# Performance work log

Hardware: AMD Instinct MI355X
Metric: run time of the kernel (lower is better)

## Reference

```python
import jax, jax.numpy as jnp
import numpy as np

N = 16384
D = 256


def setup_inputs() -> dict:
    key = jax.random.key(0)
    k1, k2, k3, k4 = jax.random.split(key, 4)
    x = jax.random.normal(k1, (N, D), dtype=jnp.float32)
    adj = jax.random.randint(k2, (N, N), 0, 2, dtype=jnp.int32)  # dense 0/1 adjacency
    W = jax.random.normal(k3, (D, D), dtype=jnp.float32) * 0.05
    b = jax.random.normal(k4, (D,), dtype=jnp.float32) * 0.05
    return {"x": x, "adj": adj, "W": W, "b": b}


def reference(x, adj, W, b):
    # neighbors of node i are columns where adj[i, :] == 1; mean-aggregate then Linear
    a = (adj == 1).astype(x.dtype)               # [N, N]
    deg = jnp.sum(a, axis=1, keepdims=True)      # [N, 1]
    agg = jnp.einsum('ij,jf->if', a, x) / deg    # mean over neighbors, [N, D]
    return agg @ W.T + b                         # nn.Linear(in, out)
```

## Files before the change

kernel.cpp:

```cpp
#include <hip/hip_runtime.h>
#include <stdint.h>

typedef __attribute__((ext_vector_type(8))) short shortx8;
typedef __attribute__((ext_vector_type(4))) float floatx4;

#define NR 16384
#define DD 256
#define SA 72
#define NSPLIT 4
#define KCH (NR / NSPLIT)
#define BK 64
#define NIT (KCH / BK)

__device__ __forceinline__ unsigned short f2bf(float f) {
    union { float f; uint32_t u; } v; v.f = f;
    uint32_t u = v.u;
    return (unsigned short)((u + 0x7FFFu + ((u >> 16) & 1u)) >> 16);
}

__global__ __launch_bounds__(256) void k_xpose(const float* __restrict__ x,
                                               unsigned short* __restrict__ xT) {
    __shared__ unsigned short t[64][72];
    const int kb = blockIdx.x * 64;
    const int nb = blockIdx.y * 64;
    const int tid = threadIdx.x;
    const int lr = tid >> 4;
    const int lc = (tid & 15) * 4;
#pragma unroll
    for (int i = 0; i < 4; ++i) {
        const int k = kb + lr + 16 * i;
        const float4 v = *(const float4*)(x + (size_t)k * DD + nb + lc);
        t[lc + 0][lr + 16 * i] = f2bf(v.x);
        t[lc + 1][lr + 16 * i] = f2bf(v.y);
        t[lc + 2][lr + 16 * i] = f2bf(v.z);
        t[lc + 3][lr + 16 * i] = f2bf(v.w);
    }
    __syncthreads();
#pragma unroll
    for (int i = 0; i < 4; ++i) {
        const int nl = lr + 16 * i;
        ushort4 o;
        o.x = t[nl][lc + 0]; o.y = t[nl][lc + 1];
        o.z = t[nl][lc + 2]; o.w = t[nl][lc + 3];
        *(ushort4*)(xT + (size_t)(nb + nl) * NR + kb + lc) = o;
    }
}

__global__ __launch_bounds__(256, 3) void k_agg(const int* __restrict__ adj,
                                                const unsigned short* __restrict__ xT,
                                                float* __restrict__ aggP,
                                                float* __restrict__ degP) {
    __shared__ __align__(16) unsigned short As[64 * SA];
    __shared__ __align__(16) unsigned short Bs[256 * SA];
    __shared__ int degs[64];

    const int tid  = threadIdx.x;
    const int wave = tid >> 6;
    const int lane = tid & 63;
    const int q    = lane >> 4;
    const int ln   = lane & 15;
    const int m0   = blockIdx.x * 64;
    const int kb0  = blockIdx.y * KCH;

    if (tid < 64) degs[tid] = 0;

    const int arow = tid >> 4;
    const int acol = (tid & 15) * 4;

    const int* ap0 = adj + (size_t)(m0 + arow) * NR + kb0 + acol;
    const int* ap1 = ap0 + (size_t)16 * NR;
    const int* ap2 = ap0 + (size_t)32 * NR;
    const int* ap3 = ap0 + (size_t)48 * NR;

    const unsigned short* bg[9];
    unsigned short* const blb = Bs + wave * 9 * 512;
#pragma unroll
    for (int j = 0; j < 9; ++j) {
        const int cid = (wave * 9 + j) * 64 + lane;
        const int n = cid / 9;
        int c = cid - n * 9; if (c > 7) c = 7;
        bg[j] = xT + (size_t)n * NR + kb0 + c * 8;
    }

    floatx4 acc[4][4] = {};
    int dacc0 = 0, dacc1 = 0, dacc2 = 0, dacc3 = 0;

    int4 a0 = *(const int4*)ap0;
    int4 a1 = *(const int4*)ap1;
    int4 a2 = *(const int4*)ap2;
    int4 a3 = *(const int4*)ap3;

    for (int it = 0; it < NIT; ++it) {
        __syncthreads();

#pragma unroll
        for (int j = 0; j < 9; ++j) {
            __builtin_amdgcn_global_load_lds(
                (const __attribute__((address_space(1))) void*)bg[j],
                (__attribute__((address_space(3))) void*)(blb + j * 512),
                16, 0, 0);
            bg[j] += BK;
        }

        ushort4 w;
        w.x = a0.x ? 0x3F80 : 0; w.y = a0.y ? 0x3F80 : 0;
        w.z = a0.z ? 0x3F80 : 0; w.w = a0.w ? 0x3F80 : 0;
        *(ushort4*)&As[(arow +  0) * SA + acol] = w;
        dacc0 += a0.x + a0.y + a0.z + a0.w;

        w.x = a1.x ? 0x3F80 : 0; w.y = a1.y ? 0x3F80 : 0;
        w.z = a1.z ? 0x3F80 : 0; w.w = a1.w ? 0x3F80 : 0;
        *(ushort4*)&As[(arow + 16) * SA + acol] = w;
        dacc1 += a1.x + a1.y + a1.z + a1.w;

        w.x = a2.x ? 0x3F80 : 0; w.y = a2.y ? 0x3F80 : 0;
        w.z = a2.z ? 0x3F80 : 0; w.w = a2.w ? 0x3F80 : 0;
        *(ushort4*)&As[(arow + 32) * SA + acol] = w;
        dacc2 += a2.x + a2.y + a2.z + a2.w;

        w.x = a3.x ? 0x3F80 : 0; w.y = a3.y ? 0x3F80 : 0;
        w.z = a3.z ? 0x3F80 : 0; w.w = a3.w ? 0x3F80 : 0;
        *(ushort4*)&As[(arow + 48) * SA + acol] = w;
        dacc3 += a3.x + a3.y + a3.z + a3.w;

        __syncthreads();

        if (it + 1 < NIT) {
            ap0 += BK; ap1 += BK; ap2 += BK; ap3 += BK;
            a0 = *(const int4*)ap0;
            a1 = *(const int4*)ap1;
            a2 = *(const int4*)ap2;
            a3 = *(const int4*)ap3;
        }

#pragma unroll
        for (int ks = 0; ks < 2; ++ks) {
            const int kk = ks * 32 + q * 8;
            shortx8 af[4], bf[4];
#pragma unroll
            for (int mt = 0; mt < 4; ++mt)
                af[mt] = *(const shortx8*)&As[(mt * 16 + ln) * SA + kk];
#pragma unroll
            for (int nt = 0; nt < 4; ++nt)
                bf[nt] = *(const shortx8*)&Bs[(wave * 64 + nt * 16 + ln) * SA + kk];
#pragma unroll
            for (int mt = 0; mt < 4; ++mt)
#pragma unroll
                for (int nt = 0; nt < 4; ++nt)
                    acc[mt][nt] = __builtin_amdgcn_mfma_f32_16x16x32_bf16(
                        af[mt], bf[nt], acc[mt][nt], 0, 0, 0);
        }
    }

    atomicAdd(&degs[arow +  0], dacc0);
    atomicAdd(&degs[arow + 16], dacc1);
    atomicAdd(&degs[arow + 32], dacc2);
    atomicAdd(&degs[arow + 48], dacc3);
    __syncthreads();
    if (tid < 64) degP[(size_t)blockIdx.y * NR + m0 + tid] = (float)degs[tid];

    float* const outb = aggP + (size_t)blockIdx.y * NR * DD;
#pragma unroll
    for (int mt = 0; mt < 4; ++mt)
#pragma unroll
        for (int nt = 0; nt < 4; ++nt)
#pragma unroll
            for (int r = 0; r < 4; ++r) {
                const int row = m0 + mt * 16 + q * 4 + r;
                const int col = wave * 64 + nt * 16 + ln;
                outb[(size_t)row * DD + col] = acc[mt][nt][r];
            }
}

__global__ __launch_bounds__(256, 2) void k_lin(const float* __restrict__ aggP,
                                                const float* __restrict__ degP,
                                                const float* __restrict__ W,
                                                const float* __restrict__ bias,
                                                float* __restrict__ out) {
    __shared__ __align__(16) unsigned short As[64 * SA];
    __shared__ __align__(16) unsigned short Bs[256 * SA];
    __shared__ float rdeg[64];
    __shared__ float bsh[256];

    const int tid  = threadIdx.x;
    const int wave = tid >> 6;
    const int lane = tid & 63;
    const int q    = lane >> 4;
    const int ln   = lane & 15;
    const int m0   = blockIdx.x * 64;

    if (tid < 64) {
        float d = 0.f;
#pragma unroll
        for (int s = 0; s < NSPLIT; ++s) d += degP[(size_t)s * NR + m0 + tid];
        rdeg[tid] = 1.0f / d;
    }
    bsh[tid] = bias[tid];

    const int arow = tid >> 4;
    const int acol = (tid & 15) * 4;

    floatx4 acc[4][4] = {};

    for (int it = 0; it < 4; ++it) {
        const int kb = it * 64;
        __syncthreads();

#pragma unroll
        for (int i = 0; i < 4; ++i) {
            const int r = arow + 16 * i;
            const size_t g = (size_t)(m0 + r) * DD + kb + acol;
            float4 p = *(const float4*)(aggP + g);
#pragma unroll
            for (int s = 1; s < NSPLIT; ++s) {
                const float4 ps = *(const float4*)(aggP + (size_t)s * NR * DD + g);
                p.x += ps.x; p.y += ps.y; p.z += ps.z; p.w += ps.w;
            }
            const float sc = rdeg[r];
            ushort4 o;
            o.x = f2bf(p.x * sc);
            o.y = f2bf(p.y * sc);
            o.z = f2bf(p.z * sc);
            o.w = f2bf(p.w * sc);
            *(ushort4*)&As[r * SA + acol] = o;
        }
#pragma unroll
        for (int i = 0; i < 16; ++i) {
            const int r = arow + 16 * i;
            const float4 w4 = *(const float4*)(W + (size_t)r * DD + kb + acol);
            ushort4 o;
            o.x = f2bf(w4.x); o.y = f2bf(w4.y);
            o.z = f2bf(w4.z); o.w = f2bf(w4.w);
            *(ushort4*)&Bs[r * SA + acol] = o;
        }
        __syncthreads();

#pragma unroll
        for (int ks = 0; ks < 2; ++ks) {
            const int kk = ks * 32 + q * 8;
            shortx8 af[4], bf[4];
#pragma unroll
            for (int mt = 0; mt < 4; ++mt)
                af[mt] = *(const shortx8*)&As[(mt * 16 + ln) * SA + kk];
#pragma unroll
            for (int nt = 0; nt < 4; ++nt)
                bf[nt] = *(const shortx8*)&Bs[(wave * 64 + nt * 16 + ln) * SA + kk];
#pragma unroll
            for (int mt = 0; mt < 4; ++mt)
#pragma unroll
                for (int nt = 0; nt < 4; ++nt)
                    acc[mt][nt] = __builtin_amdgcn_mfma_f32_16x16x32_bf16(
                        af[mt], bf[nt], acc[mt][nt], 0, 0, 0);
        }
    }

#pragma unroll
    for (int mt = 0; mt < 4; ++mt)
#pragma unroll
        for (int nt = 0; nt < 4; ++nt)
#pragma unroll
            for (int r = 0; r < 4; ++r) {
                const int row = m0 + mt * 16 + q * 4 + r;
                const int col = wave * 64 + nt * 16 + ln;
                out[(size_t)row * DD + col] = acc[mt][nt][r] + bsh[col];
            }
}

extern "C" void kernel_launch(void* const* d_in, const int* in_sizes, int n_in,
                              void* d_out, int out_size, void* d_ws, size_t ws_size,
                              hipStream_t stream) {
    const float* x    = (const float*)d_in[0];
    const int*   adj  = (const int*)d_in[1];
    const float* W    = (const float*)d_in[2];
    const float* bias = (const float*)d_in[3];
    float* out = (float*)d_out;

    unsigned short* xT  = (unsigned short*)d_ws;
    float* aggP = (float*)((char*)d_ws + (size_t)8 * 1024 * 1024);
    float* degP = (float*)((char*)d_ws + (size_t)(8 + 16 * NSPLIT) * 1024 * 1024);

    k_xpose<<<dim3(NR / 64, DD / 64), 256, 0, stream>>>(x, xT);
    k_agg<<<dim3(NR / 64, NSPLIT), 256, 0, stream>>>(adj, xT, aggP, degP);
    k_lin<<<dim3(NR / 64), 256, 0, stream>>>(aggP, degP, W, bias, out);
}
```

Before: 1.528 ms.

## Warp-specialize aggregation kernel into producer and MFMA consumer waves with double buffering

The aggregation kernel now runs 512 threads: four producer waves load adjacency and x^T tiles into double-buffered LDS, and four consumer waves run the bf16 MFMAs on the other buffer. The K step drops from 64 to 32 with narrower LDS strides. The goal is to overlap global loads and the int-to-bf16 conversion with matrix math instead of running them back to back. In exchange it issues one block barrier per smaller step, and half the waves do no MFMA work.

```diff
diff --git a/kernel.cpp b/kernel.cpp
--- a/kernel.cpp
+++ b/kernel.cpp
@@ -6,11 +6,13 @@
 
 #define NR 16384
 #define DD 256
-#define SA 72
 #define NSPLIT 4
 #define KCH (NR / NSPLIT)
-#define BK 64
+#define BK 32
 #define NIT (KCH / BK)
+#define SB 40
+#define SAS 40
+#define SA 72
 
 __device__ __forceinline__ unsigned short f2bf(float f) {
     union { float f; uint32_t u; } v; v.f = f;
@@ -46,103 +48,110 @@
     }
 }
 
-__global__ __launch_bounds__(256, 3) void k_agg(const int* __restrict__ adj,
+__global__ __launch_bounds__(512, 2) void k_agg(const int* __restrict__ adj,
                                                 const unsigned short* __restrict__ xT,
                                                 float* __restrict__ aggP,
                                                 float* __restrict__ degP) {
-    __shared__ __align__(16) unsigned short As[64 * SA];
-    __shared__ __align__(16) unsigned short Bs[256 * SA];
+    __shared__ __align__(16) unsigned short Bs[2][256 * SB];
+    __shared__ __align__(16) unsigned short As[2][64 * SAS];
     __shared__ int degs[64];
 
     const int tid  = threadIdx.x;
     const int wave = tid >> 6;
     const int lane = tid & 63;
-    const int q    = lane >> 4;
-    const int ln   = lane & 15;
     const int m0   = blockIdx.x * 64;
     const int kb0  = blockIdx.y * KCH;
 
     if (tid < 64) degs[tid] = 0;
 
-    const int arow = tid >> 4;
-    const int acol = (tid & 15) * 4;
-
-    const int* ap0 = adj + (size_t)(m0 + arow) * NR + kb0 + acol;
-    const int* ap1 = ap0 + (size_t)16 * NR;
-    const int* ap2 = ap0 + (size_t)32 * NR;
-    const int* ap3 = ap0 + (size_t)48 * NR;
-
-    const unsigned short* bg[9];
-    unsigned short* const blb = Bs + wave * 9 * 512;
-#pragma unroll
-    for (int j = 0; j < 9; ++j) {
-        const int cid = (wave * 9 + j) * 64 + lane;
-        const int n = cid / 9;
-        int c = cid - n * 9; if (c > 7) c = 7;
-        bg[j] = xT + (size_t)n * NR + kb0 + c * 8;
-    }
-
+    const bool prod = (wave < 4);
+
+    const int prow = tid >> 2;
+    const int pc   = tid & 3;
+    const int* apn = adj + (size_t)(m0 + prow) * NR + kb0 + pc * 8;
+    const unsigned short* bg[5];
+    {
+#pragma unroll
+        for (int j = 0; j < 5; ++j) {
+            const int cid = (wave * 5 + j) * 64 + lane;
+            const int row = cid / 5;
+            int sub = cid - row * 5; if (sub > 3) sub = 3;
+            bg[j] = xT + (size_t)row * NR + kb0 + sub * 8;
+        }
+    }
+    int4 ra[2][2];
+    int dacc = 0;
+
+    const int cw = wave - 4;
+    const int q  = lane >> 4;
+    const int ln = lane & 15;
     floatx4 acc[4][4] = {};
-    int dacc0 = 0, dacc1 = 0, dacc2 = 0, dacc3 = 0;
-
-    int4 a0 = *(const int4*)ap0;
-    int4 a1 = *(const int4*)ap1;
-    int4 a2 = *(const int4*)ap2;
-    int4 a3 = *(const int4*)ap3;
-
-    for (int it = 0; it < NIT; ++it) {
-        __syncthreads();
-
-#pragma unroll
-        for (int j = 0; j < 9; ++j) {
+
+    if (prod) {
+#pragma unroll
+        for (int j = 0; j < 5; ++j) {
             __builtin_amdgcn_global_load_lds(
                 (const __attribute__((address_space(1))) void*)bg[j],
-                (__attribute__((address_space(3))) void*)(blb + j * 512),
+                (__attribute__((address_space(3))) void*)((char*)Bs[0] + (wave * 5 + j) * 1024),
                 16, 0, 0);
             bg[j] += BK;
         }
-
-        ushort4 w;
-        w.x = a0.x ? 0x3F80 : 0; w.y = a0.y ? 0x3F80 : 0;
-        w.z = a0.z ? 0x3F80 : 0; w.w = a0.w ? 0x3F80 : 0;
-        *(ushort4*)&As[(arow +  0) * SA + acol] = w;
-        dacc0 += a0.x + a0.y + a0.z + a0.w;
-
-        w.x = a1.x ? 0x3F80 : 0; w.y = a1.y ? 0x3F80 : 0;
-        w.z = a1.z ? 0x3F80 : 0; w.w = a1.w ? 0x3F80 : 0;
-        *(ushort4*)&As[(arow + 16) * SA + acol] = w;
-        dacc1 += a1.x + a1.y + a1.z + a1.w;
-
-        w.x = a2.x ? 0x3F80 : 0; w.y = a2.y ? 0x3F80 : 0;
-        w.z = a2.z ? 0x3F80 : 0; w.w = a2.w ? 0x3F80 : 0;
-        *(ushort4*)&As[(arow + 32) * SA + acol] = w;
-        dacc2 += a2.x + a2.y + a2.z + a2.w;
-
-        w.x = a3.x ? 0x3F80 : 0; w.y = a3.y ? 0x3F80 : 0;
-        w.z = a3.z ? 0x3F80 : 0; w.w = a3.w ? 0x3F80 : 0;
-        *(ushort4*)&As[(arow + 48) * SA + acol] = w;
-        dacc3 += a3.x + a3.y + a3.z + a3.w;
-
-        __syncthreads();
-
-        if (it + 1 < NIT) {
-            ap0 += BK; ap1 += BK; ap2 += BK; ap3 += BK;
-            a0 = *(const int4*)ap0;
-            a1 = *(const int4*)ap1;
-            a2 = *(const int4*)ap2;
-            a3 = *(const int4*)ap3;
-        }
-
-#pragma unroll
-        for (int ks = 0; ks < 2; ++ks) {
-            const int kk = ks * 32 + q * 8;
+        ra[0][0] = *(const int4*)(apn);
+        ra[0][1] = *(const int4*)(apn + 4);
+        {
+            const int4 c0 = ra[0][0], c1 = ra[0][1];
+            ushort4 w0, w1;
+            w0.x = c0.x ? 0x3F80 : 0; w0.y = c0.y ? 0x3F80 : 0;
+            w0.z = c0.z ? 0x3F80 : 0; w0.w = c0.w ? 0x3F80 : 0;
+            w1.x = c1.x ? 0x3F80 : 0; w1.y = c1.y ? 0x3F80 : 0;
+            w1.z = c1.z ? 0x3F80 : 0; w1.w = c1.w ? 0x3F80 : 0;
+            *(ushort4*)&As[0][prow * SAS + pc * 8 + 0] = w0;
+            *(ushort4*)&As[0][prow * SAS + pc * 8 + 4] = w1;
+            dacc += c0.x + c0.y + c0.z + c0.w + c1.x + c1.y + c1.z + c1.w;
+        }
+        ra[1][0] = *(const int4*)(apn + BK);
+        ra[1][1] = *(const int4*)(apn + BK + 4);
+        apn += 2 * BK;
+    }
+    __syncthreads();
+
+    int buf = 0;
+    for (int it = 0; it < NIT; ++it) {
+        if (prod) {
+            if (it + 1 < NIT) {
+                const int nb = buf ^ 1;
+#pragma unroll
+                for (int j = 0; j < 5; ++j) {
+                    __builtin_amdgcn_global_load_lds(
+                        (const __attribute__((address_space(1))) void*)bg[j],
+                        (__attribute__((address_space(3))) void*)((char*)Bs[nb] + (wave * 5 + j) * 1024),
+                        16, 0, 0);
+                    bg[j] += BK;
+                }
+                const int rs = (it + 1) & 1;
+                const int4 c0 = ra[rs][0], c1 = ra[rs][1];
+                ushort4 w0, w1;
+                w0.x = c0.x ? 0x3F80 : 0; w0.y = c0.y ? 0x3F80 : 0;
+                w0.z = c0.z ? 0x3F80 : 0; w0.w = c0.w ? 0x3F80 : 0;
+                w1.x = c1.x ? 0x3F80 : 0; w1.y = c1.y ? 0x3F80 : 0;
+                w1.z = c1.z ? 0x3F80 : 0; w1.w = c1.w ? 0x3F80 : 0;
+                *(ushort4*)&As[nb][prow * SAS + pc * 8 + 0] = w0;
+                *(ushort4*)&As[nb][prow * SAS + pc * 8 + 4] = w1;
+                dacc += c0.x + c0.y + c0.z + c0.w + c1.x + c1.y + c1.z + c1.w;
+                if (it + 2 < NIT) {
+                    ra[rs ^ 1][0] = *(const int4*)(apn);
+                    ra[rs ^ 1][1] = *(const int4*)(apn + 4);
+                    apn += BK;
+                }
+            }
+        } else {
             shortx8 af[4], bf[4];
 #pragma unroll
             for (int mt = 0; mt < 4; ++mt)
-                af[mt] = *(const shortx8*)&As[(mt * 16 + ln) * SA + kk];
+                af[mt] = *(const shortx8*)&As[buf][(mt * 16 + ln) * SAS + q * 8];
 #pragma unroll
             for (int nt = 0; nt < 4; ++nt)
-                bf[nt] = *(const shortx8*)&Bs[(wave * 64 + nt * 16 + ln) * SA + kk];
+                bf[nt] = *(const shortx8*)&Bs[buf][(cw * 64 + nt * 16 + ln) * SB + q * 8];
 #pragma unroll
             for (int mt = 0; mt < 4; ++mt)
 #pragma unroll
@@ -150,26 +159,27 @@
                     acc[mt][nt] = __builtin_amdgcn_mfma_f32_16x16x32_bf16(
                         af[mt], bf[nt], acc[mt][nt], 0, 0, 0);
         }
-    }
-
-    atomicAdd(&degs[arow +  0], dacc0);
-    atomicAdd(&degs[arow + 16], dacc1);
-    atomicAdd(&degs[arow + 32], dacc2);
-    atomicAdd(&degs[arow + 48], dacc3);
+        __syncthreads();
+        buf ^= 1;
+    }
+
+    if (prod) atomicAdd(&degs[prow], dacc);
     __syncthreads();
     if (tid < 64) degP[(size_t)blockIdx.y * NR + m0 + tid] = (float)degs[tid];
 
-    float* const outb = aggP + (size_t)blockIdx.y * NR * DD;
-#pragma unroll
-    for (int mt = 0; mt < 4; ++mt)
-#pragma unroll
-        for (int nt = 0; nt < 4; ++nt)
-#pragma unroll
-            for (int r = 0; r < 4; ++r) {
-                const int row = m0 + mt * 16 + q * 4 + r;
-                const int col = wave * 64 + nt * 16 + ln;
-                outb[(size_t)row * DD + col] = acc[mt][nt][r];
-            }
+    if (!prod) {
+        float* const outb = aggP + (size_t)blockIdx.y * NR * DD;
+#pragma unroll
+        for (int mt = 0; mt < 4; ++mt)
+#pragma unroll
+            for (int nt = 0; nt < 4; ++nt)
+#pragma unroll
+                for (int r = 0; r < 4; ++r) {
+                    const int row = m0 + mt * 16 + q * 4 + r;
+                    const int col = cw * 64 + nt * 16 + ln;
+                    outb[(size_t)row * DD + col] = acc[mt][nt][r];
+                }
+    }
 }
 
 __global__ __launch_bounds__(256, 2) void k_lin(const float* __restrict__ aggP,
@@ -280,6 +290,6 @@
     float* degP = (float*)((char*)d_ws + (size_t)(8 + 16 * NSPLIT) * 1024 * 1024);
 
     k_xpose<<<dim3(NR / 64, DD / 64), 256, 0, stream>>>(x, xT);
-    k_agg<<<dim3(NR / 64, NSPLIT), 256, 0, stream>>>(adj, xT, aggP, degP);
+    k_agg<<<dim3(NR / 64, NSPLIT), 512, 0, stream>>>(adj, xT, aggP, degP);
     k_lin<<<dim3(NR / 64), 256, 0, stream>>>(aggP, degP, W, bias, out);
 }
```

Measured after the change: 2.112 ms. 1.38x slower.

## Double-buffer aggregation tiles with async LDS loads and raw int adjacency staging

Applied to the files above, without the earlier changes.

Restructures the aggregation GEMM main loop to double-buffer both the adjacency and the transposed-feature tiles in LDS using direct global-to-LDS loads, with BK reduced to 32. The adjacency tile is now staged as raw int32 with an XOR swizzle, and the 0/1-to-bf16 conversion and degree counting move into the fragment-load stage (wave 0 only counts degree). This removes the register round-trip and the extra barrier per iteration and overlaps the next tile's loads with MFMA work. In exchange it doubles the LDS footprint per buffer for adjacency (int vs bf16), which may reduce occupancy, and adds conversion ALU work in every wave.

```diff
diff --git a/kernel.cpp b/kernel.cpp
--- a/kernel.cpp
+++ b/kernel.cpp
@@ -6,11 +6,11 @@
 
 #define NR 16384
 #define DD 256
-#define SA 72
 #define NSPLIT 4
 #define KCH (NR / NSPLIT)
-#define BK 64
+#define BK 32
 #define NIT (KCH / BK)
+#define SA 72
 
 __device__ __forceinline__ unsigned short f2bf(float f) {
     union { float f; uint32_t u; } v; v.f = f;
@@ -50,8 +50,8 @@
                                                 const unsigned short* __restrict__ xT,
                                                 float* __restrict__ aggP,
                                                 float* __restrict__ degP) {
-    __shared__ __align__(16) unsigned short As[64 * SA];
-    __shared__ __align__(16) unsigned short Bs[256 * SA];
+    __shared__ __align__(16) int            AsI[2][64 * 32];
+    __shared__ __align__(16) unsigned short Bs [2][256 * 32];
     __shared__ int degs[64];
 
     const int tid  = threadIdx.x;
@@ -64,98 +64,104 @@
 
     if (tid < 64) degs[tid] = 0;
 
-    const int arow = tid >> 4;
-    const int acol = (tid & 15) * 4;
-
-    const int* ap0 = adj + (size_t)(m0 + arow) * NR + kb0 + acol;
-    const int* ap1 = ap0 + (size_t)16 * NR;
-    const int* ap2 = ap0 + (size_t)32 * NR;
-    const int* ap3 = ap0 + (size_t)48 * NR;
-
-    const unsigned short* bg[9];
-    unsigned short* const blb = Bs + wave * 9 * 512;
-#pragma unroll
-    for (int j = 0; j < 9; ++j) {
-        const int cid = (wave * 9 + j) * 64 + lane;
-        const int n = cid / 9;
-        int c = cid - n * 9; if (c > 7) c = 7;
-        bg[j] = xT + (size_t)n * NR + kb0 + c * 8;
+    const int* srcA[2];
+#pragma unroll
+    for (int j = 0; j < 2; ++j) {
+        const int L = (wave * 2 + j) * 64 + lane;
+        const int r = L >> 3;
+        const int pp = L & 7;
+        const int p  = pp ^ (r & 7);
+        srcA[j] = adj + (size_t)(m0 + r) * NR + kb0 + p * 4;
+    }
+    const unsigned short* srcB[4];
+#pragma unroll
+    for (int j = 0; j < 4; ++j) {
+        const int L = (wave * 4 + j) * 64 + lane;
+        const int n = L >> 2;
+        const int pb = L & 3;
+        srcB[j] = xT + (size_t)n * NR + kb0 + pb * 8;
     }
 
     floatx4 acc[4][4] = {};
-    int dacc0 = 0, dacc1 = 0, dacc2 = 0, dacc3 = 0;
-
-    int4 a0 = *(const int4*)ap0;
-    int4 a1 = *(const int4*)ap1;
-    int4 a2 = *(const int4*)ap2;
-    int4 a3 = *(const int4*)ap3;
-
+    int dacc[4] = {0, 0, 0, 0};
+
+    const int pp0 = (2 * q) ^ (ln & 7);
+    const int pp1 = pp0 ^ 1;
+
+#pragma unroll
+    for (int j = 0; j < 2; ++j) {
+        __builtin_amdgcn_global_load_lds(
+            (const __attribute__((address_space(1))) void*)srcA[j],
+            (__attribute__((address_space(3))) void*)(AsI[0] + (wave * 2 + j) * 256),
+            16, 0, 0);
+        srcA[j] += BK;
+    }
+#pragma unroll
+    for (int j = 0; j < 4; ++j) {
+        __builtin_amdgcn_global_load_lds(
+            (const __attribute__((address_space(1))) void*)srcB[j],
+            (__attribute__((address_space(3))) void*)(Bs[0] + (wave * 4 + j) * 512),
+            16, 0, 0);
+        srcB[j] += BK;
+    }
+    __syncthreads();
+
+    int buf = 0;
     for (int it = 0; it < NIT; ++it) {
+        if (it + 1 < NIT) {
+            const int nb = buf ^ 1;
+#pragma unroll
+            for (int j = 0; j < 2; ++j) {
+                __builtin_amdgcn_global_load_lds(
+                    (const __attribute__((address_space(1))) void*)srcA[j],
+                    (__attribute__((address_space(3))) void*)(AsI[nb] + (wave * 2 + j) * 256),
+                    16, 0, 0);
+                srcA[j] += BK;
+            }
+#pragma unroll
+            for (int j = 0; j < 4; ++j) {
+                __builtin_amdgcn_global_load_lds(
+                    (const __attribute__((address_space(1))) void*)srcB[j],
+                    (__attribute__((address_space(3))) void*)(Bs[nb] + (wave * 4 + j) * 512),
+                    16, 0, 0);
+                srcB[j] += BK;
+            }
+        }
+
+        shortx8 af[4], bf[4];
+#pragma unroll
+        for (int mt = 0; mt < 4; ++mt) {
+            const int* base = &AsI[buf][(mt * 16 + ln) * 32];
+            const int4 c0 = *(const int4*)(base + pp0 * 4);
+            const int4 c1 = *(const int4*)(base + pp1 * 4);
+            union { shortx8 v; uint32_t u[4]; } A;
+            A.u[0] = (c0.x ? 0x3F80u : 0u) | (c0.y ? 0x3F800000u : 0u);
+            A.u[1] = (c0.z ? 0x3F80u : 0u) | (c0.w ? 0x3F800000u : 0u);
+            A.u[2] = (c1.x ? 0x3F80u : 0u) | (c1.y ? 0x3F800000u : 0u);
+            A.u[3] = (c1.z ? 0x3F80u : 0u) | (c1.w ? 0x3F800000u : 0u);
+            af[mt] = A.v;
+            if (wave == 0)
+                dacc[mt] += c0.x + c0.y + c0.z + c0.w + c1.x + c1.y + c1.z + c1.w;
+        }
+#pragma unroll
+        for (int nt = 0; nt < 4; ++nt)
+            bf[nt] = *(const shortx8*)&Bs[buf][(wave * 64 + nt * 16 + ln) * 32 + q * 8];
+#pragma unroll
+        for (int mt = 0; mt < 4; ++mt)
+#pragma unroll
+            for (int nt = 0; nt < 4; ++nt)
+                acc[mt][nt] = __builtin_amdgcn_mfma_f32_16x16x32_bf16(
+                    af[mt], bf[nt], acc[mt][nt], 0, 0, 0);
+
         __syncthreads();
-
-#pragma unroll
-        for (int j = 0; j < 9; ++j) {
-            __builtin_amdgcn_global_load_lds(
-                (const __attribute__((address_space(1))) void*)bg[j],
-                (__attribute__((address_space(3))) void*)(blb + j * 512),
-                16, 0, 0);
-            bg[j] += BK;
-        }
-
-        ushort4 w;
-        w.x = a0.x ? 0x3F80 : 0; w.y = a0.y ? 0x3F80 : 0;
-        w.z = a0.z ? 0x3F80 : 0; w.w = a0.w ? 0x3F80 : 0;
-        *(ushort4*)&As[(arow +  0) * SA + acol] = w;
-        dacc0 += a0.x + a0.y + a0.z + a0.w;
-
-        w.x = a1.x ? 0x3F80 : 0; w.y = a1.y ? 0x3F80 : 0;
-        w.z = a1.z ? 0x3F80 : 0; w.w = a1.w ? 0x3F80 : 0;
-        *(ushort4*)&As[(arow + 16) * SA + acol] = w;
-        dacc1 += a1.x + a1.y + a1.z + a1.w;
-
-        w.x = a2.x ? 0x3F80 : 0; w.y = a2.y ? 0x3F80 : 0;
-        w.z = a2.z ? 0x3F80 : 0; w.w = a2.w ? 0x3F80 : 0;
-        *(ushort4*)&As[(arow + 32) * SA + acol] = w;
-        dacc2 += a2.x + a2.y + a2.z + a2.w;
-
-        w.x = a3.x ? 0x3F80 : 0; w.y = a3.y ? 0x3F80 : 0;
-        w.z = a3.z ? 0x3F80 : 0; w.w = a3.w ? 0x3F80 : 0;
-        *(ushort4*)&As[(arow + 48) * SA + acol] = w;
-        dacc3 += a3.x + a3.y + a3.z + a3.w;
-
-        __syncthreads();
-
-        if (it + 1 < NIT) {
-            ap0 += BK; ap1 += BK; ap2 += BK; ap3 += BK;
-            a0 = *(const int4*)ap0;
-            a1 = *(const int4*)ap1;
-            a2 = *(const int4*)ap2;
-            a3 = *(const int4*)ap3;
-        }
-
-#pragma unroll
-        for (int ks = 0; ks < 2; ++ks) {
-            const int kk = ks * 32 + q * 8;
-            shortx8 af[4], bf[4];
-#pragma unroll
-            for (int mt = 0; mt < 4; ++mt)
-                af[mt] = *(const shortx8*)&As[(mt * 16 + ln) * SA + kk];
-#pragma unroll
-            for (int nt = 0; nt < 4; ++nt)
-                bf[nt] = *(const shortx8*)&Bs[(wave * 64 + nt * 16 + ln) * SA + kk];
-#pragma unroll
-            for (int mt = 0; mt < 4; ++mt)
-#pragma unroll
-                for (int nt = 0; nt < 4; ++nt)
-                    acc[mt][nt] = __builtin_amdgcn_mfma_f32_16x16x32_bf16(
-                        af[mt], bf[nt], acc[mt][nt], 0, 0, 0);
-        }
-    }
-
-    atomicAdd(&degs[arow +  0], dacc0);
-    atomicAdd(&degs[arow + 16], dacc1);
-    atomicAdd(&degs[arow + 32], dacc2);
-    atomicAdd(&degs[arow + 48], dacc3);
+        buf ^= 1;
+    }
+
+    if (wave == 0) {
+#pragma unroll
+        for (int mt = 0; mt < 4; ++mt)
+            atomicAdd(&degs[mt * 16 + ln], dacc[mt]);
+    }
     __syncthreads();
     if (tid < 64) degP[(size_t)blockIdx.y * NR + m0 + tid] = (float)degs[tid];
 
```

After: 1.589 ms. +3.9%, slower.
